# Kernel optimization log

Hardware: AMD Instinct MI355X
Metric: run time of the kernel (lower is better)

The kernel has to match this reference:

```python
import jax, jax.numpy as jnp
import numpy as np
import math

N, E, D, H, EH, DEPTH = 50000, 800000, 128, 128, 16, 3
RATIO = 0.5
BN_SCALE = 1.0 / math.sqrt(1.0 + 1e-5)  # eval-mode BatchNorm1d: running mean 0, var 1
NEG_SLOPE = 0.01  # leaky_relu default


def setup_inputs() -> dict:
    key = jax.random.key(0)
    ks = jax.random.split(key, 16)
    s = lambda k, shape: jax.random.normal(k, shape, dtype=jnp.float32) * 0.05
    return {
        "x": jax.random.normal(ks[0], (N, D), dtype=jnp.float32),
        "edge_index": jax.random.randint(ks[1], (2, E), 0, N, dtype=jnp.int32),
        "edge_attr": jax.random.uniform(ks[2], (E, EH), dtype=jnp.float32),
        "We_w": s(ks[3], (EH, 1)), "We_b": s(ks[4], (1,)),
        "Wdown": s(ks[5], (DEPTH + 1, H, H)), "bdown": s(ks[6], (DEPTH + 1, H)),
        "Wpool": s(ks[7], (DEPTH, H)),
        "Wup": s(ks[8], (DEPTH, H, H)), "bup": s(ks[9], (DEPTH, H)),
        "gnorm": 1.0 + s(ks[10], (DEPTH + 1, H)), "bnorm": s(ks[11], (DEPTH + 1, H)),
        "Wr": s(ks[12], (D, D)), "br": s(ks[13], (D,)),
        "gr": 1.0 + s(ks[14], (D,)), "brn": s(ks[15], (D,)),
    }


def _bn(x, g, b):
    # eval-mode BatchNorm1d with running_mean=0, running_var=1
    return x * (g * BN_SCALE) + b


def _lrelu(x):
    return jnp.where(x > 0, x, NEG_SLOPE * x)


def _gcn(x, src, dst, w, W, b, fill):
    # PyG GCNConv: add self-loops (fill=1.0, improved -> 2.0), symmetric norm
    n = x.shape[0]
    h = x @ W  # [n, H]
    deg = jax.ops.segment_sum(w, dst, num_segments=n) + fill
    dinv = jax.lax.rsqrt(deg)
    coef = dinv[src] * w * dinv[dst]  # [E]
    agg = jax.ops.segment_sum(coef[:, None] * h[src], dst, num_segments=n)
    return agg + (fill / deg)[:, None] * h + b  # self-loop norm = fill/deg


def _topk_pool(x, src, dst, w, p, k):
    # PyG TopKPooling: score = tanh(x.p/||p||), keep top-k, scale kept x by score,
    # filter edges to kept nodes (masked edges kept at fixed length with weight 0)
    n = x.shape[0]
    score = jnp.tanh((x @ p) / jnp.linalg.norm(p))
    vals, perm = jax.lax.top_k(score, k)
    xp = x[perm] * vals[:, None]
    pos = jnp.full((n,), -1, dtype=jnp.int32).at[perm].set(jnp.arange(k, dtype=jnp.int32))
    ns, nd = pos[src], pos[dst]
    valid = (ns >= 0) & (nd >= 0)
    return (xp, jnp.where(valid, ns, 0), jnp.where(valid, nd, 0),
            jnp.where(valid, w, 0.0), perm)


def reference(x, edge_index, edge_attr, We_w, We_b, Wdown, bdown, Wpool, Wup, bup,
              gnorm, bnorm, Wr, br, gr, brn):
    src, dst = edge_index[0], edge_index[1]
    # edge embedding + min/max normalization
    ew = edge_attr @ We_w[:, 0] + We_b[0]  # [E]
    ew = ew - jnp.min(ew)
    ew = ew / (jnp.max(ew) + 1e-7)
    h = _bn(x, gnorm[0], bnorm[0])
    h = _lrelu(_gcn(h, src, dst, ew, Wdown[0], bdown[0], 1.0))
    xs, es, perms = [h], [(src, dst, ew)], []
    for i in range(DEPTH):
        k = int(math.ceil(RATIO * h.shape[0]))
        h, src, dst, ew, perm = _topk_pool(h, src, dst, ew, Wpool[i], k)
        h = _bn(h, gnorm[i + 1], bnorm[i + 1])
        h = _gcn(h, src, dst, ew, Wdown[i + 1], bdown[i + 1], 1.0)
        if i < DEPTH - 1:
            h = _lrelu(h)
            xs.append(h)
            es.append((src, dst, ew))
        perms.append(perm)
    for i in range(DEPTH):
        j = DEPTH - 1 - i
        res = xs[j]
        src, dst, ew = es[j]
        up = jnp.zeros_like(res).at[perms[j]].set(h)  # scatter unpool
        h = _gcn(res + up, src, dst, ew, Wup[i], bup[i], 2.0)  # improved=True -> fill 2
        if i < DEPTH - 1:
            h = _lrelu(h)
    g = jnp.sum(h, axis=0, keepdims=True)  # global_add_pool, single graph
    g = g @ Wr + br
    return _bn(g, gr, brn)
```

## Files before the change

kernel.cpp:

```cpp
#include <hip/hip_runtime.h>
#include <math.h>

#define N0   50000
#define E0   800000
#define HD   128
#define EHD  16
#define KP1  25000
#define KP2  12500
#define KP3  6250
#define BN_SCALE 0.9999950000374997f
#define NEG_SLOPE 0.01f
#define E1C  400000
#define E2C  120000
#define E3C  40000
#define NBE  782
#define CSB  782

#define NBIN   782
#define SBCAP  448
#define OVFCAP 4096

typedef int   vi4 __attribute__((ext_vector_type(4)));
typedef float vf4 __attribute__((ext_vector_type(4)));

__device__ __forceinline__ unsigned fenc(float f) {
    unsigned u = __float_as_uint(f);
    return (u & 0x80000000u) ? ~u : (u | 0x80000000u);
}
__device__ __forceinline__ unsigned packbf2(float a, float b) {
    unsigned ua = __float_as_uint(a);
    unsigned ub = __float_as_uint(b);
    ua = (ua + 0x7FFFu + ((ua >> 16) & 1u)) >> 16;
    ub = (ub + 0x7FFFu + ((ub >> 16) & 1u)) >> 16;
    return ua | (ub << 16);
}
__device__ __forceinline__ void bf8_fma(float* acc, uint4 h, float c) {
    acc[0] += c * __uint_as_float(h.x << 16);
    acc[1] += c * __uint_as_float(h.x & 0xFFFF0000u);
    acc[2] += c * __uint_as_float(h.y << 16);
    acc[3] += c * __uint_as_float(h.y & 0xFFFF0000u);
    acc[4] += c * __uint_as_float(h.z << 16);
    acc[5] += c * __uint_as_float(h.z & 0xFFFF0000u);
    acc[6] += c * __uint_as_float(h.w << 16);
    acc[7] += c * __uint_as_float(h.w & 0xFFFF0000u);
}

__global__ void k_edge_ew(const float* __restrict__ ea, const float* __restrict__ Ww,
                          const float* __restrict__ Wb, float* __restrict__ ew,
                          float2* __restrict__ partials, int E) {
    int e = blockIdx.x * 256 + threadIdx.x;
    float mn = 3.4e38f, mx = -3.4e38f;
    if (e < E) {
        const float4* a4 = (const float4*)(ea + (size_t)e * EHD);
        float s = Wb[0];
        #pragma unroll
        for (int q = 0; q < 4; ++q) {
            float4 a = a4[q];
            s += a.x * Ww[q*4+0] + a.y * Ww[q*4+1] + a.z * Ww[q*4+2] + a.w * Ww[q*4+3];
        }
        ew[e] = s;
        mn = s; mx = s;
    }
    #pragma unroll
    for (int off = 32; off > 0; off >>= 1) {
        mn = fminf(mn, __shfl_xor(mn, off));
        mx = fmaxf(mx, __shfl_xor(mx, off));
    }
    __shared__ float smn[4], smx[4];
    int lane = threadIdx.x & 63, wid = threadIdx.x >> 6;
    if (lane == 0) { smn[wid] = mn; smx[wid] = mx; }
    __syncthreads();
    if (threadIdx.x == 0) {
        float a = fminf(fminf(smn[0], smn[1]), fminf(smn[2], smn[3]));
        float b = fmaxf(fmaxf(smx[0], smx[1]), fmaxf(smx[2], smx[3]));
        partials[blockIdx.x] = make_float2(a, b);
    }
}

__global__ void __launch_bounds__(1024)
k_reduce_mm(const float2* __restrict__ partials, int nb, float* __restrict__ mmv) {
    float mn = 3.4e38f, mx = -3.4e38f;
    for (int i = threadIdx.x; i < nb; i += 1024) {
        float2 t = partials[i];
        mn = fminf(mn, t.x); mx = fmaxf(mx, t.y);
    }
    #pragma unroll
    for (int off = 32; off > 0; off >>= 1) {
        mn = fminf(mn, __shfl_xor(mn, off));
        mx = fmaxf(mx, __shfl_xor(mx, off));
    }
    __shared__ float smn[16], smx[16];
    int lane = threadIdx.x & 63, wid = threadIdx.x >> 6;
    if (lane == 0) { smn[wid] = mn; smx[wid] = mx; }
    __syncthreads();
    if (threadIdx.x == 0) {
        for (int w = 1; w < 16; ++w) { mn = fminf(mn, smn[w]); mx = fmaxf(mx, smx[w]); }
        mmv[0] = mn; mmv[1] = mx;
    }
}

__global__ void __launch_bounds__(256)
k_ew_norm_stage(float* __restrict__ ew, const float* __restrict__ mmv,
                const int* __restrict__ src, const int* __restrict__ dst,
                int* __restrict__ subCnt, uint2* __restrict__ staging,
                int4* __restrict__ ovfList, int* __restrict__ ovfCnt, int E) {
    unsigned xcd;
    asm volatile("s_getreg_b32 %0, hwreg(HW_REG_XCC_ID)" : "=s"(xcd));
    int e = blockIdx.x * 256 + threadIdx.x;
    if (e >= E) return;
    float mn = mmv[0];
    float sc = 1.0f / ((mmv[1] - mn) + 1e-7f);
    float w = (ew[e] - mn) * sc;
    ew[e] = w;
    if (w == 0.0f) return;
    int d = dst[e];
    int s = src[e];
    int sb = (int)xcd * NBIN + (d >> 6);
    int slot = atomicAdd(&subCnt[sb], 1);
    if (slot < SBCAP) {
        staging[(size_t)sb * SBCAP + slot] =
            make_uint2((unsigned)s | ((unsigned)(d & 63) << 16), __float_as_uint(w));
    } else {
        int o = atomicAdd(ovfCnt, 1);
        if (o < OVFCAP) ovfList[o] = make_int4(s, d, __float_as_int(w), 0);
    }
}

__global__ void __launch_bounds__(1024)
k_bin_scan(const int* __restrict__ subCnt, int* __restrict__ binBase,
           int* __restrict__ rowptrEnd) {
    int t = threadIdx.x;
    int v = 0;
    if (t < NBIN) {
        #pragma unroll
        for (int x = 0; x < 8; ++x) v += subCnt[x * NBIN + t];
    }
    int lane = t & 63, wid = t >> 6;
    int xs = v;
    #pragma unroll
    for (int off = 1; off < 64; off <<= 1) {
        int y = __shfl_up(xs, off);
        if (lane >= off) xs += y;
    }
    __shared__ int wsum[16];
    if (lane == 63) wsum[wid] = xs;
    __syncthreads();
    int wb = 0;
    for (int w = 0; w < wid; ++w) wb += wsum[w];
    int excl = wb + xs - v;
    if (t < NBIN) binBase[t] = excl;
    if (t == NBIN - 1) rowptrEnd[0] = excl + v;
}

#define GT_ROWS 64
__global__ void __launch_bounds__(256)
k_gemm128(const float* __restrict__ A, const float* __restrict__ W,
          unsigned* __restrict__ Cb, int n,
          const float* __restrict__ gs, const float* __restrict__ gb,
          const float* __restrict__ up_h, const int* __restrict__ up_pos) {
    __shared__ float As[GT_ROWS][132];
    int tid = threadIdx.x;
    int row0 = blockIdx.x * GT_ROWS;
    int maxr = n - row0;
    {
        #pragma unroll
        for (int it = 0; it < 8; ++it) {
            int idx = it * 256 + tid;
            int r = idx >> 5, q = idx & 31;
            float4 v = make_float4(0.f, 0.f, 0.f, 0.f);
            if (r < maxr) {
                v = ((const float4*)(A + (size_t)(row0 + r) * HD))[q];
                if (up_pos) {
                    int sl = up_pos[row0 + r];
                    if (sl >= 0) {
                        float4 u = ((const float4*)(up_h + (size_t)sl * HD))[q];
                        v.x += u.x; v.y += u.y; v.z += u.z; v.w += u.w;
                    }
                }
                if (gs) {
                    float4 g4 = ((const float4*)gs)[q];
                    float4 b4 = ((const float4*)gb)[q];
                    v.x = v.x * (g4.x * BN_SCALE) + b4.x;
                    v.y = v.y * (g4.y * BN_SCALE) + b4.y;
                    v.z = v.z * (g4.z * BN_SCALE) + b4.z;
                    v.w = v.w * (g4.w * BN_SCALE) + b4.w;
                }
            }
            *(float4*)&As[r][q * 4] = v;
        }
    }
    __syncthreads();
    int cg = tid & 31;
    int rg = tid >> 5;
    float4 acc[8];
    #pragma unroll
    for (int j = 0; j < 8; ++j) acc[j] = make_float4(0.f, 0.f, 0.f, 0.f);
    const float4* W4 = (const float4*)W;
    #pragma unroll 4
    for (int k = 0; k < HD; k += 4) {
        float4 w0 = W4[(k + 0) * 32 + cg];
        float4 w1 = W4[(k + 1) * 32 + cg];
        float4 w2 = W4[(k + 2) * 32 + cg];
        float4 w3 = W4[(k + 3) * 32 + cg];
        #pragma unroll
        for (int jj = 0; jj < 4; ++jj) {
            float4 a = *(const float4*)&As[4 * rg + jj][k];
            acc[jj].x += a.x * w0.x + a.y * w1.x + a.z * w2.x + a.w * w3.x;
            acc[jj].y += a.x * w0.y + a.y * w1.y + a.z * w2.y + a.w * w3.y;
            acc[jj].z += a.x * w0.z + a.y * w1.z + a.z * w2.z + a.w * w3.z;
            acc[jj].w += a.x * w0.w + a.y * w1.w + a.z * w2.w + a.w * w3.w;
        }
        #pragma unroll
        for (int jj = 0; jj < 4; ++jj) {
            float4 a = *(const float4*)&As[32 + 4 * rg + jj][k];
            acc[4 + jj].x += a.x * w0.x + a.y * w1.x + a.z * w2.x + a.w * w3.x;
            acc[4 + jj].y += a.x * w0.y + a.y * w1.y + a.z * w2.y + a.w * w3.y;
            acc[4 + jj].z += a.x * w0.z + a.y * w1.z + a.z * w2.z + a.w * w3.z;
            acc[4 + jj].w += a.x * w0.w + a.y * w1.w + a.z * w2.w + a.w * w3.w;
        }
    }
    #pragma unroll
    for (int jj = 0; jj < 4; ++jj) {
        int r = 4 * rg + jj;
        if (r < maxr) {
            uint2 pk = make_uint2(packbf2(acc[jj].x, acc[jj].y), packbf2(acc[jj].z, acc[jj].w));
            ((uint2*)(Cb + (size_t)(row0 + r) * 64))[cg] = pk;
        }
    }
    #pragma unroll
    for (int jj = 0; jj < 4; ++jj) {
        int r = 32 + 4 * rg + jj;
        if (r < maxr) {
            uint2 pk = make_uint2(packbf2(acc[4+jj].x, acc[4+jj].y), packbf2(acc[4+jj].z, acc[4+jj].w));
            ((uint2*)(Cb + (size_t)(row0 + r) * 64))[cg] = pk;
        }
    }
}

__global__ void k_sum_scan(const int* __restrict__ cnt, int* __restrict__ bsum, int n,
                           int* __restrict__ totalOut, unsigned* __restrict__ dctr) {
    int base = blockIdx.x * 1024;
    int s = 0;
    #pragma unroll
    for (int it = 0; it < 4; ++it) {
        int i = base + it * 256 + threadIdx.x;
        if (i < n) s += cnt[i];
    }
    __shared__ int ws[4];
    __shared__ int lastFlag;
    int lane = threadIdx.x & 63, wid = threadIdx.x >> 6;
    #pragma unroll
    for (int off = 32; off > 0; off >>= 1) s += __shfl_down(s, off);
    if (lane == 0) ws[wid] = s;
    __syncthreads();
    if (threadIdx.x == 0) {
        __hip_atomic_store(&bsum[blockIdx.x], ws[0] + ws[1] + ws[2] + ws[3],
                           __ATOMIC_RELAXED, __HIP_MEMORY_SCOPE_AGENT);
        unsigned prev = __hip_atomic_fetch_add(dctr, 1u, __ATOMIC_ACQ_REL, __HIP_MEMORY_SCOPE_AGENT);
        lastFlag = (prev == gridDim.x - 1);
    }
    __syncthreads();
    if (!lastFlag) return;
    if (threadIdx.x < 64) {
        int nb = gridDim.x;
        int t = threadIdx.x;
        int v = (t < nb) ? __hip_atomic_load(&bsum[t], __ATOMIC_RELAXED, __HIP_MEMORY_SCOPE_AGENT) : 0;
        int x = v;
        #pragma unroll
        for (int off = 1; off < 64; off <<= 1) {
            int y = __shfl_up(x, off);
            if (t >= off) x += y;
        }
        if (t < nb) bsum[t] = x - v;
        if (t == nb - 1) totalOut[0] = x;
    }
    if (threadIdx.x == 0)
        __hip_atomic_store(dctr, 0u, __ATOMIC_RELAXED, __HIP_MEMORY_SCOPE_AGENT);
}

__global__ void k_chunk_scan(const int* __restrict__ cnt, const int* __restrict__ bo,
                             int* __restrict__ rowptr, int* __restrict__ cursor, int n) {
    __shared__ int wsum[4];
    __shared__ int running;
    int base = blockIdx.x * 1024;
    if (threadIdx.x == 0) running = bo[blockIdx.x];
    __syncthreads();
    int lane = threadIdx.x & 63, wid = threadIdx.x >> 6;
    #pragma unroll
    for (int it = 0; it < 4; ++it) {
        int i = base + it * 256 + threadIdx.x;
        int v = (i < n) ? cnt[i] : 0;
        int x = v;
        #pragma unroll
        for (int off = 1; off < 64; off <<= 1) {
            int y = __shfl_up(x, off);
            if (lane >= off) x += y;
        }
        if (lane == 63) wsum[wid] = x;
        __syncthreads();
        int wb = 0;
        for (int w = 0; w < wid; ++w) wb += wsum[w];
        int excl = running + wb + x - v;
        if (i < n) { rowptr[i] = excl; cursor[i] = excl; }
        __syncthreads();
        if (threadIdx.x == 0) running += wsum[0] + wsum[1] + wsum[2] + wsum[3];
        __syncthreads();
    }
}

__global__ void k_csr_fill(const int* __restrict__ src, const int* __restrict__ dst,
                           const float* __restrict__ w, int* __restrict__ cursor,
                           int2* __restrict__ csr,
                           const int* __restrict__ EinPtr, int EinImm) {
    int Ein = EinPtr ? EinPtr[0] : EinImm;
    int e = blockIdx.x * 256 + threadIdx.x;
    if (e >= Ein) return;
    float wv = w[e];
    if (wv == 0.0f) return;
    int slot = atomicAdd(&cursor[dst[e]], 1);
    csr[slot] = make_int2(src[e], __float_as_int(wv));
}

__global__ void __launch_bounds__(256)
k_binB_r(const int* __restrict__ binBase, const int* __restrict__ subCnt,
         const uint2* __restrict__ staging, int2* __restrict__ csr,
         int* __restrict__ cursor, float* __restrict__ sumW,
         int* __restrict__ rowptr, int n) {
    __shared__ int   lhist[64];
    __shared__ int   lcur[64];
    __shared__ float lw[64];
    __shared__ int2  img[2048];
    __shared__ int   segc[8];
    __shared__ int   totalSh;
    int b = blockIdx.x;
    int v0 = b * 64;
    int base = binBase[b];
    if (threadIdx.x < 64) { lhist[threadIdx.x] = 0; lw[threadIdx.x] = 0.f; }
    if (threadIdx.x < 8) segc[threadIdx.x] = min(subCnt[threadIdx.x * NBIN + b], SBCAP);
    __syncthreads();
    #pragma unroll 1
    for (int x = 0; x < 8; ++x) {
        int cnt = segc[x];
        const uint2* st = staging + (size_t)(x * NBIN + b) * SBCAP;
        for (int i = threadIdx.x; i < cnt; i += 256) {
            uint2 en = st[i];
            int dloc = (en.x >> 16) & 63;
            atomicAdd(&lhist[dloc], 1);
            atomicAdd(&lw[dloc], __uint_as_float(en.y));
        }
    }
    __syncthreads();
    if (threadIdx.x < 64) {
        int c = lhist[threadIdx.x];
        int xs = c;
        #pragma unroll
        for (int off = 1; off < 64; off <<= 1) {
            int y = __shfl_up(xs, off);
            if (threadIdx.x >= (unsigned)off) xs += y;
        }
        int excl = xs - c;
        lcur[threadIdx.x] = excl;
        int v = v0 + threadIdx.x;
        if (v < n) { rowptr[v] = base + excl; sumW[v] = lw[threadIdx.x]; }
        if (threadIdx.x == 63) totalSh = xs;
    }
    __syncthreads();
    #pragma unroll 1
    for (int x = 0; x < 8; ++x) {
        int cnt = segc[x];
        const uint2* st = staging + (size_t)(x * NBIN + b) * SBCAP;
        for (int i = threadIdx.x; i < cnt; i += 256) {
            uint2 en = st[i];
            int dloc = (en.x >> 16) & 63;
            int slot = atomicAdd(&lcur[dloc], 1);
            if (slot < 2048) img[slot] = make_int2((int)(en.x & 0xFFFFu), (int)en.y);
        }
    }
    __syncthreads();
    int total = min(totalSh, 2048);
    for (int i = threadIdx.x; i < total; i += 256)
        csr[base + i] = img[i];
    if (threadIdx.x < 64) {
        int v = v0 + threadIdx.x;
        if (v < n) cursor[v] = base + lcur[threadIdx.x];
    }
}

__global__ void k_binOvf(const int4* __restrict__ ovfList, const int* __restrict__ ovfCnt,
                         int* __restrict__ cursor, int2* __restrict__ csr,
                         float* __restrict__ sumW) {
    int cnt = min(ovfCnt[0], OVFCAP);
    for (int i = threadIdx.x; i < cnt; i += 256) {
        int4 e = ovfList[i];
        int slot = atomicAdd(&cursor[e.y], 1);
        csr[slot] = make_int2(e.x, e.z);
        atomicAdd(&sumW[e.y], __int_as_float(e.z));
    }
}

__global__ void k_deg_dinv(const int* __restrict__ rowptr, const int2* __restrict__ csr,
                           float fill, float* __restrict__ deg, float* __restrict__ dinv, int n) {
    int v = blockIdx.x * 256 + threadIdx.x;
    if (v >= n) return;
    float s = fill;
    int rs = rowptr[v], re = rowptr[v + 1];
    for (int j = rs; j < re; ++j) s += __int_as_float(csr[j].y);
    deg[v] = s;
    dinv[v] = rsqrtf(s);
}

__global__ void k_deg_dinv_d(const float* __restrict__ sumW, float fill,
                             float* __restrict__ deg, float* __restrict__ dinv, int n) {
    int v = blockIdx.x * 256 + threadIdx.x;
    if (v >= n) return;
    float s = fill + sumW[v];
    deg[v] = s;
    dinv[v] = rsqrtf(s);
}

__global__ void __launch_bounds__(256)
k_gcn_gather(const int* __restrict__ rowptr, const int2* __restrict__ csr,
             const float* __restrict__ deg, const float* __restrict__ dinv,
             const unsigned* __restrict__ hWb,
             const float* __restrict__ bias,
             float fill, int n, int lrelu, float* __restrict__ out) {
    int v = blockIdx.x * 4 + (threadIdx.x >> 6);
    int lane = threadIdx.x & 63;
    if (v >= n) return;
    int rs = rowptr[v], re = rowptr[v + 1];
    float dv = dinv[v];
    int quarter = lane >> 4;
    int qi = lane & 15;
    float acc[8];
    #pragma unroll
    for (int i = 0; i < 8; ++i) acc[i] = 0.f;
    for (int base = rs; base < re; base += 64) {
        int idx = base + lane;
        int s_r = 0; float c_r = 0.f;
        if (idx < re) {
            int2 ent = csr[idx];
            s_r = ent.x;
            c_r = dinv[s_r] * __int_as_float(ent.y) * dv;
        }
        int cnt = min(64, re - base);
        int groups = cnt >> 2;
        int t = 0;
        for (; t + 1 < groups; t += 2) {
            int j0 = 4 * t + quarter, j1 = j0 + 4;
            int   s0 = __shfl(s_r, j0); float c0 = __shfl(c_r, j0);
            int   s1 = __shfl(s_r, j1); float c1 = __shfl(c_r, j1);
            uint4 h0 = ((const uint4*)(hWb + (size_t)s0 * 64))[qi];
            uint4 h1 = ((const uint4*)(hWb + (size_t)s1 * 64))[qi];
            bf8_fma(acc, h0, c0);
            bf8_fma(acc, h1, c1);
        }
        for (; t < groups; ++t) {
            int j = 4 * t + quarter;
            int s = __shfl(s_r, j); float c = __shfl(c_r, j);
            uint4 h = ((const uint4*)(hWb + (size_t)s * 64))[qi];
            bf8_fma(acc, h, c);
        }
        int rem = cnt & 3;
        if (quarter < rem) {
            int j = groups * 4 + quarter;
            int s = __shfl(s_r, j); float c = __shfl(c_r, j);
            uint4 h = ((const uint4*)(hWb + (size_t)s * 64))[qi];
            bf8_fma(acc, h, c);
        }
    }
    #pragma unroll
    for (int i = 0; i < 8; ++i) {
        acc[i] += __shfl_xor(acc[i], 16);
        acc[i] += __shfl_xor(acc[i], 32);
    }
    if (quarter == 0) {
        uint4 hs = ((const uint4*)(hWb + (size_t)v * 64))[qi];
        float sc = fill / deg[v];
        float hv[8];
        hv[0] = __uint_as_float(hs.x << 16); hv[1] = __uint_as_float(hs.x & 0xFFFF0000u);
        hv[2] = __uint_as_float(hs.y << 16); hv[3] = __uint_as_float(hs.y & 0xFFFF0000u);
        hv[4] = __uint_as_float(hs.z << 16); hv[5] = __uint_as_float(hs.z & 0xFFFF0000u);
        hv[6] = __uint_as_float(hs.w << 16); hv[7] = __uint_as_float(hs.w & 0xFFFF0000u);
        float4 b0 = ((const float4*)bias)[2 * qi];
        float4 b1 = ((const float4*)bias)[2 * qi + 1];
        float o[8];
        o[0] = acc[0] + sc * hv[0] + b0.x;
        o[1] = acc[1] + sc * hv[1] + b0.y;
        o[2] = acc[2] + sc * hv[2] + b0.z;
        o[3] = acc[3] + sc * hv[3] + b0.w;
        o[4] = acc[4] + sc * hv[4] + b1.x;
        o[5] = acc[5] + sc * hv[5] + b1.y;
        o[6] = acc[6] + sc * hv[6] + b1.z;
        o[7] = acc[7] + sc * hv[7] + b1.w;
        if (lrelu) {
            #pragma unroll
            for (int i = 0; i < 8; ++i) o[i] = (o[i] > 0.f) ? o[i] : NEG_SLOPE * o[i];
        }
        float4* orow = (float4*)(out + (size_t)v * HD);
        orow[2 * qi]     = make_float4(o[0], o[1], o[2], o[3]);
        orow[2 * qi + 1] = make_float4(o[4], o[5], o[6], o[7]);
    }
}

__global__ void k_score(const float* __restrict__ x, const float* __restrict__ p,
                        float* __restrict__ score, int n, int* __restrict__ selws) {
    for (int i = blockIdx.x * 256 + threadIdx.x; i < 5120; i += gridDim.x * 256) selws[i] = 0;
    int lane = threadIdx.x & 63;
    float pv0 = p[lane], pv1 = p[lane + 64];
    float ps = pv0 * pv0 + pv1 * pv1;
    #pragma unroll
    for (int off = 32; off > 0; off >>= 1) ps += __shfl_xor(ps, off);
    float rnorm = 1.0f / sqrtf(ps);
    int node = blockIdx.x * 4 + (threadIdx.x >> 6);
    if (node >= n) return;
    const float* row = x + (size_t)node * HD;
    float s = row[lane] * pv0 + row[lane + 64] * pv1;
    #pragma unroll
    for (int off = 32; off > 0; off >>= 1) s += __shfl_xor(s, off);
    if (lane == 0) score[node] = tanhf(s * rnorm);
}

__global__ void __launch_bounds__(256)
k_histpick(const float* __restrict__ score, int n, int pass,
           unsigned* __restrict__ prefix, int* __restrict__ hist,
           int kImm, const int* __restrict__ remIn, int* __restrict__ remOut,
           unsigned* __restrict__ doneCtr) {
    __shared__ int lh[2048];
    int nbins = (pass == 2) ? 1024 : 2048;
    for (int i = threadIdx.x; i < nbins; i += 256) lh[i] = 0;
    __syncthreads();
    unsigned pfx = (pass != 0) ? prefix[0] : 0u;
    int stride = gridDim.x * 256;
    for (int i = blockIdx.x * 256 + threadIdx.x; i < n; i += stride) {
        unsigned u = fenc(score[i]);
        int bin; bool ok;
        if (pass == 0)      { bin = u >> 21;            ok = true; }
        else if (pass == 1) { bin = (u >> 10) & 2047;   ok = ((u >> 21) == (pfx >> 21)); }
        else                { bin = u & 1023;           ok = ((u >> 10) == (pfx >> 10)); }
        if (ok) atomicAdd(&lh[bin], 1);
    }
    __syncthreads();
    for (int i = threadIdx.x; i < nbins; i += 256) {
        int c = lh[i];
        if (c) __hip_atomic_fetch_add(&hist[i], c, __ATOMIC_RELAXED, __HIP_MEMORY_SCOPE_AGENT);
    }
    __syncthreads();
    __shared__ int lastFlag;
    if (threadIdx.x == 0) {
        unsigned prev = __hip_atomic_fetch_add(doneCtr, 1u, __ATOMIC_ACQ_REL, __HIP_MEMORY_SCOPE_AGENT);
        lastFlag = (prev == gridDim.x - 1);
    }
    __syncthreads();
    if (!lastFlag) return;
    __shared__ int wsum[4];
    int k = remIn ? remIn[0] : kImm;
    int t = threadIdx.x;
    int per = nbins >> 8;
    int hi = nbins - t * per, lo = hi - per;
    int s = 0;
    for (int b = lo; b < hi; ++b)
        s += __hip_atomic_load(&hist[b], __ATOMIC_RELAXED, __HIP_MEMORY_SCOPE_AGENT);
    int lane = t & 63, wid = t >> 6;
    int x = s;
    #pragma unroll
    for (int off = 1; off < 64; off <<= 1) {
        int y = __shfl_up(x, off);
        if (lane >= off) x += y;
    }
    if (lane == 63) wsum[wid] = x;
    __syncthreads();
    int wb = 0;
    for (int w = 0; w < wid; ++w) wb += wsum[w];
    int excl = wb + x - s;
    if (k > excl && k <= excl + s) {
        int cum = excl;
        int shift = (pass == 0) ? 21 : (pass == 1) ? 10 : 0;
        for (int b = hi - 1; b >= lo; --b) {
            int h = __hip_atomic_load(&hist[b], __ATOMIC_RELAXED, __HIP_MEMORY_SCOPE_AGENT);
            if (k <= cum + h) {
                unsigned base = (pass == 0) ? 0u : prefix[0];
                prefix[0] = base | ((unsigned)b << shift);
                remOut[0] = k - cum;
                break;
            }
            cum += h;
        }
    }
    __syncthreads();
    if (threadIdx.x == 0)
        __hip_atomic_store(doneCtr, 0u, __ATOMIC_RELAXED, __HIP_MEMORY_SCOPE_AGENT);
}

__global__ void k_cmp_countscan(const float* __restrict__ score, int n,
                                const unsigned* __restrict__ prefix,
                                int* __restrict__ bgt, int* __restrict__ beq,
                                unsigned* __restrict__ dctr) {
    unsigned T = prefix[0];
    int base = blockIdx.x * 1024;
    int gt = 0, eq = 0;
    #pragma unroll
    for (int it = 0; it < 4; ++it) {
        int i = base + it * 256 + threadIdx.x;
        if (i < n) {
            unsigned u = fenc(score[i]);
            gt += (u > T); eq += (u == T);
        }
    }
    __shared__ int sg[4], se[4];
    __shared__ int lastFlag;
    int lane = threadIdx.x & 63, wid = threadIdx.x >> 6;
    #pragma unroll
    for (int off = 32; off > 0; off >>= 1) { gt += __shfl_down(gt, off); eq += __shfl_down(eq, off); }
    if (lane == 0) { sg[wid] = gt; se[wid] = eq; }
    __syncthreads();
    if (threadIdx.x == 0) {
        __hip_atomic_store(&bgt[blockIdx.x], sg[0] + sg[1] + sg[2] + sg[3],
                           __ATOMIC_RELAXED, __HIP_MEMORY_SCOPE_AGENT);
        __hip_atomic_store(&beq[blockIdx.x], se[0] + se[1] + se[2] + se[3],
                           __ATOMIC_RELAXED, __HIP_MEMORY_SCOPE_AGENT);
        unsigned prev = __hip_atomic_fetch_add(dctr, 1u, __ATOMIC_ACQ_REL, __HIP_MEMORY_SCOPE_AGENT);
        lastFlag = (prev == gridDim.x - 1);
    }
    __syncthreads();
    if (!lastFlag) return;
    if (threadIdx.x < 64) {
        int nb = gridDim.x;
        int t = threadIdx.x;
        int va = (t < nb) ? __hip_atomic_load(&bgt[t], __ATOMIC_RELAXED, __HIP_MEMORY_SCOPE_AGENT) : 0;
        int vb = (t < nb) ? __hip_atomic_load(&beq[t], __ATOMIC_RELAXED, __HIP_MEMORY_SCOPE_AGENT) : 0;
        int xa = va, xb = vb;
        #pragma unroll
        for (int off = 1; off < 64; off <<= 1) {
            int ya = __shfl_up(xa, off), yb = __shfl_up(xb, off);
            if (t >= off) { xa += ya; xb += yb; }
        }
        if (t < nb) { bgt[t] = xa - va; beq[t] = xb - vb; }
    }
    if (threadIdx.x == 0)
        __hip_atomic_store(dctr, 0u, __ATOMIC_RELAXED, __HIP_MEMORY_SCOPE_AGENT);
}

__global__ void k_cmp_assign(const float* __restrict__ score, int n, int kcap,
                             const unsigned* __restrict__ prefix,
                             const int* __restrict__ selTies,
                             const int* __restrict__ bgt, const int* __restrict__ beq,
                             int* __restrict__ pos, int* __restrict__ perm,
                             float* __restrict__ vals) {
    unsigned T = prefix[0];
    int tiesNeed = selTies[0];
    __shared__ int wgt[4], weq[4];
    __shared__ int rgt, req;
    int base = blockIdx.x * 1024;
    if (threadIdx.x == 0) { rgt = bgt[blockIdx.x]; req = beq[blockIdx.x]; }
    __syncthreads();
    int lane = threadIdx.x & 63, wid = threadIdx.x >> 6;
    #pragma unroll
    for (int it = 0; it < 4; ++it) {
        int i = base + it * 256 + threadIdx.x;
        bool in = i < n;
        float sc = in ? score[i] : 0.f;
        unsigned u = in ? fenc(sc) : 0u;
        bool g = in && (u > T);
        bool e = in && (u == T);
        unsigned long long mg = __ballot(g), me = __ballot(e);
        int lgt = __popcll(mg & ((1ull << lane) - 1ull));
        int leq = __popcll(me & ((1ull << lane) - 1ull));
        if (lane == 0) { wgt[wid] = __popcll(mg); weq[wid] = __popcll(me); }
        __syncthreads();
        int wbg = 0, wbe = 0;
        for (int w = 0; w < wid; ++w) { wbg += wgt[w]; wbe += weq[w]; }
        int gtRank = rgt + wbg + lgt;
        int tieRank = req + wbe + leq;
        if (in) {
            int slot = -1;
            if (g) slot = gtRank + min(tieRank, tiesNeed);
            else if (e && tieRank < tiesNeed) slot = gtRank + tieRank;
            if (slot >= kcap) slot = -1;
            pos[i] = slot;
            if (slot >= 0) { perm[slot] = i; vals[slot] = sc; }
        }
        __syncthreads();
        if (threadIdx.x == 0) {
            rgt += wgt[0] + wgt[1] + wgt[2] + wgt[3];
            req += weq[0] + weq[1] + weq[2] + weq[3];
        }
        __syncthreads();
    }
}

__global__ void k_pool_bn(const float* __restrict__ x, const int* __restrict__ perm,
                          const float* __restrict__ vals, const float* __restrict__ g,
                          const float* __restrict__ b, float* __restrict__ out, int k) {
    int idx = blockIdx.x * 256 + threadIdx.x;
    if (idx >= k * HD) return;
    int slot = idx >> 7, c = idx & 127;
    int v = perm[slot];
    out[idx] = (x[(size_t)v * HD + c] * vals[slot]) * (g[c] * BN_SCALE) + b[c];
}

__global__ void k_ecompact_countscan(const int* __restrict__ src, const int* __restrict__ dst,
                                     const float* __restrict__ w, const int* __restrict__ pos,
                                     const int* __restrict__ EinPtr, int EinImm, int kNodes,
                                     int* __restrict__ bsumE, int* __restrict__ ecntOut,
                                     int* __restrict__ cnt, unsigned* __restrict__ dctr) {
    int Ein = EinPtr ? EinPtr[0] : EinImm;
    for (int i = blockIdx.x * 256 + threadIdx.x; i < kNodes; i += gridDim.x * 256) cnt[i] = 0;
    int base = blockIdx.x * 1024;
    int c = 0;
    #pragma unroll
    for (int it = 0; it < 4; ++it) {
        int e = base + it * 256 + threadIdx.x;
        if (e < Ein) {
            float wv = w[e];
            if (wv != 0.0f && pos[src[e]] >= 0 && pos[dst[e]] >= 0) ++c;
        }
    }
    __shared__ int ws[4];
    __shared__ int lastFlag;
    int lane = threadIdx.x & 63, wid = threadIdx.x >> 6;
    #pragma unroll
    for (int off = 32; off > 0; off >>= 1) c += __shfl_down(c, off);
    if (lane == 0) ws[wid] = c;
    __syncthreads();
    if (threadIdx.x == 0) {
        __hip_atomic_store(&bsumE[blockIdx.x], ws[0] + ws[1] + ws[2] + ws[3],
                           __ATOMIC_RELAXED, __HIP_MEMORY_SCOPE_AGENT);
        unsigned prev = __hip_atomic_fetch_add(dctr, 1u, __ATOMIC_ACQ_REL, __HIP_MEMORY_SCOPE_AGENT);
        lastFlag = (prev == gridDim.x - 1);
    }
    __syncthreads();
    if (!lastFlag) return;
    {
        __shared__ int wtot[4];
        int nb = gridDim.x;
        int t = threadIdx.x;
        int i0 = t * 4;
        int v0 = (i0 + 0 < nb) ? __hip_atomic_load(&bsumE[i0 + 0], __ATOMIC_RELAXED, __HIP_MEMORY_SCOPE_AGENT) : 0;
        int v1 = (i0 + 1 < nb) ? __hip_atomic_load(&bsumE[i0 + 1], __ATOMIC_RELAXED, __HIP_MEMORY_SCOPE_AGENT) : 0;
        int v2 = (i0 + 2 < nb) ? __hip_atomic_load(&bsumE[i0 + 2], __ATOMIC_RELAXED, __HIP_MEMORY_SCOPE_AGENT) : 0;
        int v3 = (i0 + 3 < nb) ? __hip_atomic_load(&bsumE[i0 + 3], __ATOMIC_RELAXED, __HIP_MEMORY_SCOPE_AGENT) : 0;
        int tot = v0 + v1 + v2 + v3;
        int x2 = tot;
        #pragma unroll
        for (int off = 1; off < 64; off <<= 1) {
            int y = __shfl_up(x2, off);
            if (lane >= off) x2 += y;
        }
        if (lane == 63) wtot[wid] = x2;
        __syncthreads();
        int wb = 0;
        for (int q = 0; q < wid; ++q) wb += wtot[q];
        int excl = wb + x2 - tot;
        if (i0 + 0 < nb) bsumE[i0 + 0] = excl;
        if (i0 + 1 < nb) bsumE[i0 + 1] = excl + v0;
        if (i0 + 2 < nb) bsumE[i0 + 2] = excl + v0 + v1;
        if (i0 + 3 < nb) bsumE[i0 + 3] = excl + v0 + v1 + v2;
        if (t == 255) ecntOut[0] = wtot[0] + wtot[1] + wtot[2] + wtot[3];
    }
    __syncthreads();
    if (threadIdx.x == 0)
        __hip_atomic_store(dctr, 0u, __ATOMIC_RELAXED, __HIP_MEMORY_SCOPE_AGENT);
}

__global__ void k_ecompact_assign(const int* __restrict__ src, const int* __restrict__ dst,
                                  const float* __restrict__ w, const int* __restrict__ pos,
                                  const int* __restrict__ EinPtr, int EinImm,
                                  const int* __restrict__ bsumE,
                                  int* __restrict__ nsrc, int* __restrict__ ndst,
                                  float* __restrict__ nw, int* __restrict__ cnt) {
    int Ein = EinPtr ? EinPtr[0] : EinImm;
    __shared__ int wcnt[4];
    __shared__ int running;
    if (threadIdx.x == 0) running = bsumE[blockIdx.x];
    __syncthreads();
    int base = blockIdx.x * 1024;
    int lane = threadIdx.x & 63, wid = threadIdx.x >> 6;
    #pragma unroll
    for (int it = 0; it < 4; ++it) {
        int e = base + it * 256 + threadIdx.x;
        bool valid = false; int ns = 0, nd = 0; float wv = 0.f;
        if (e < Ein) {
            wv = w[e];
            if (wv != 0.0f) {
                ns = pos[src[e]]; nd = pos[dst[e]];
                valid = (ns >= 0) && (nd >= 0);
            }
        }
        unsigned long long m = __ballot(valid);
        int r = __popcll(m & ((1ull << lane) - 1ull));
        if (lane == 0) wcnt[wid] = __popcll(m);
        __syncthreads();
        int wb = 0;
        for (int w2 = 0; w2 < wid; ++w2) wb += wcnt[w2];
        if (valid) {
            int slot = running + wb + r;
            nsrc[slot] = ns; ndst[slot] = nd; nw[slot] = wv;
            atomicAdd(&cnt[nd], 1);
        }
        __syncthreads();
        if (threadIdx.x == 0) running += wcnt[0] + wcnt[1] + wcnt[2] + wcnt[3];
        __syncthreads();
    }
}

__global__ void __launch_bounds__(256)
k_colsum_part(const float* __restrict__ h, float* __restrict__ cpart, int n) {
    int c = threadIdx.x & 127;
    int rh = threadIdx.x >> 7;
    int r0 = blockIdx.x * 64;
    int r1 = min(n, r0 + 64);
    float local = 0.f;
    for (int r = r0 + rh; r < r1; r += 2) local += h[(size_t)r * HD + c];
    __shared__ float sh[256];
    sh[threadIdx.x] = local;
    __syncthreads();
    if (threadIdx.x < 128) cpart[(size_t)blockIdx.x * HD + c] = sh[c] + sh[c + 128];
}

__global__ void __launch_bounds__(1024)
k_colsum_final(const float* __restrict__ cpart, int nb,
               const float* __restrict__ Wr, const float* __restrict__ br,
               const float* __restrict__ gr, const float* __restrict__ brn,
               float* __restrict__ out) {
    __shared__ float gsh[HD];
    int c = threadIdx.x & 127;
    int seg = threadIdx.x >> 7;
    float local = 0.f;
    for (int b = seg; b < nb; b += 8) local += cpart[(size_t)b * HD + c];
    __shared__ float sh[1024];
    sh[threadIdx.x] = local;
    __syncthreads();
    if (threadIdx.x < 128) {
        float s = 0.f;
        #pragma unroll
        for (int q = 0; q < 8; ++q) s += sh[c + q * 128];
        gsh[c] = s;
    }
    __syncthreads();
    if (threadIdx.x < 128) {
        float s = br[c];
        for (int k = 0; k < HD; ++k) s += gsh[k] * Wr[k * HD + c];
        out[c] = s * (gr[c] * BN_SCALE) + brn[c];
    }
}

extern "C" void kernel_launch(void* const* d_in, const int* in_sizes, int n_in,
                              void* d_out, int out_size, void* d_ws, size_t ws_size,
                              hipStream_t stream) {
    const float* x     = (const float*)d_in[0];
    const int*   ei    = (const int*)d_in[1];
    const float* eattr = (const float*)d_in[2];
    const float* We_w  = (const float*)d_in[3];
    const float* We_b  = (const float*)d_in[4];
    const float* Wdown = (const float*)d_in[5];
    const float* bdown = (const float*)d_in[6];
    const float* Wpool = (const float*)d_in[7];
    const float* Wup   = (const float*)d_in[8];
    const float* bup   = (const float*)d_in[9];
    const float* gnorm = (const float*)d_in[10];
    const float* bnorm = (const float*)d_in[11];
    const float* Wr    = (const float*)d_in[12];
    const float* br    = (const float*)d_in[13];
    const float* gr    = (const float*)d_in[14];
    const float* brn   = (const float*)d_in[15];
    const int* src0 = ei;
    const int* dst0 = ei + E0;
    float* out = (float*)d_out;

    char* p = (char*)d_ws;
    auto alloc = [&](size_t bytes) -> void* {
        void* r = (void*)p;
        p += (bytes + 255) & ~(size_t)255;
        return r;
    };
    float* ew0  = (float*)alloc(E0 * 4);
    int* src1 = (int*)alloc(E1C * 4); int* dst1 = (int*)alloc(E1C * 4); float* ew1 = (float*)alloc(E1C * 4);
    int* src2 = (int*)alloc(E2C * 4); int* dst2 = (int*)alloc(E2C * 4); float* ew2 = (float*)alloc(E2C * 4);
    int* src3 = (int*)alloc(E3C * 4); int* dst3 = (int*)alloc(E3C * 4); float* ew3 = (float*)alloc(E3C * 4);
    float* hbuf = (float*)alloc((size_t)N0 * HD * 4);
    unsigned* hWb = (unsigned*)alloc((size_t)N0 * 64 * 4);
    float* tmp  = (float*)alloc((size_t)N0 * HD * 4);
    float* xs0  = (float*)alloc((size_t)N0 * HD * 4);
    float* xs1  = (float*)alloc((size_t)KP1 * HD * 4);
    float* xs2  = (float*)alloc((size_t)KP2 * HD * 4);
    float* deg   = (float*)alloc(N0 * 4);
    float* dinv  = (float*)alloc(N0 * 4);
    float* sumW0 = (float*)alloc(N0 * 4);
    float* score = (float*)alloc(N0 * 4);
    int*   pos1  = (int*)alloc(N0 * 4);
    int*   pos2  = (int*)alloc(N0 * 4);
    int*   pos3  = (int*)alloc(N0 * 4);
    float* vals  = (float*)alloc(KP1 * 4);
    int* perm1 = (int*)alloc(KP1 * 4);
    int* perm2 = (int*)alloc(KP2 * 4);
    int* perm3 = (int*)alloc(KP3 * 4);
    int* rowptr0 = (int*)alloc((N0 + 1) * 4);
    int* rowptr1 = (int*)alloc((KP1 + 1) * 4);
    int* rowptr2 = (int*)alloc((KP2 + 1) * 4);
    int* rowptr3 = (int*)alloc((KP3 + 1) * 4);
    int2* csrP0 = (int2*)alloc((size_t)E0 * 8);
    int2* csrP1 = (int2*)alloc((size_t)E1C * 8);
    int2* csrP2 = (int2*)alloc((size_t)E2C * 8);
    int2* csrP3 = (int2*)alloc((size_t)E3C * 8);
    int* cnt    = (int*)alloc(N0 * 4);
    int* cursor = (int*)alloc(N0 * 4);
    int* selws  = (int*)alloc(5120 * 4);
    int* hist0 = selws;
    int* hist1 = selws + 2048;
    int* hist2 = selws + 4096;
    int* bgt    = (int*)alloc(64 * 4);
    int* beq    = (int*)alloc(64 * 4);
    int* bsum   = (int*)alloc(64 * 4);
    int* bsumE  = (int*)alloc(1024 * 4);
    float2* partials = (float2*)alloc(((E0 + 255) / 256) * 8);
    float* cpart = (float*)alloc((size_t)CSB * HD * 4);
    float* mmv       = (float*)alloc(64);
    unsigned* ctrws  = (unsigned*)alloc(64 * 4);
    unsigned* dctrS  = ctrws + 0;
    unsigned* dctrH  = ctrws + 8;
    unsigned* dctrC  = ctrws + 16;
    unsigned* dctrE  = ctrws + 24;
    unsigned* prefix = (unsigned*)alloc(64);
    int* rem0        = (int*)alloc(64);
    int* rem1        = (int*)alloc(64);
    int* tiesN       = (int*)alloc(64);
    int* ecnt1       = (int*)alloc(64);
    int* ecnt2       = (int*)alloc(64);
    int* ecnt3       = (int*)alloc(64);
    int* subCnt      = (int*)alloc((8 * NBIN + 64) * 4);
    int* ovfCnt      = subCnt + 8 * NBIN;
    int* binBase     = (int*)alloc((NBIN + 1) * 4);
    int4* ovfList    = (int4*)alloc((size_t)OVFCAP * 16);
    uint2* staging   = (uint2*)tmp;

    const int EB = (E0 + 255) / 256;

    auto build_csr = [&](const int* esrc, const int* edst, const float* eww, int n,
                         int* rowptr, int2* csrP,
                         const int* EinPtr, int EinImm, int gridE) {
        int nb = (n + 1023) / 1024;
        k_sum_scan<<<nb, 256, 0, stream>>>(cnt, bsum, n, rowptr + n, dctrS);
        k_chunk_scan<<<nb, 256, 0, stream>>>(cnt, bsum, rowptr, cursor, n);
        k_csr_fill<<<gridE, 256, 0, stream>>>(esrc, edst, eww, cursor, csrP, EinPtr, EinImm);
    };

    auto run_gcn = [&](const float* hin, const int* rowptr, const int2* csrP,
                       const float* sumW,
                       const float* W, const float* bias, float fill, int n, int lrelu,
                       float* outbuf, const float* bn_g, const float* bn_b,
                       const float* up_h, const int* up_pos) {
        k_gemm128<<<(n + GT_ROWS - 1) / GT_ROWS, 256, 0, stream>>>(hin, W, hWb, n, bn_g, bn_b, up_h, up_pos);
        if (sumW)
            k_deg_dinv_d<<<(n + 255) / 256, 256, 0, stream>>>(sumW, fill, deg, dinv, n);
        else
            k_deg_dinv<<<(n + 255) / 256, 256, 0, stream>>>(rowptr, csrP, fill, deg, dinv, n);
        k_gcn_gather<<<(n + 3) / 4, 256, 0, stream>>>(rowptr, csrP, deg, dinv, hWb,
                                                      bias, fill, n, lrelu, outbuf);
    };

    auto run_pool = [&](const float* xin, int n, int k, const float* pvec,
                        const float* g, const float* b,
                        const int* esrc_in, const int* edst_in, const float* ew_in,
                        const int* EinPtr, int EinImm,
                        int* pos, int* perm,
                        int* esrc_out, int* edst_out, float* ew_out, int* ecntOut) {
        int nb = (n + 1023) / 1024;
        k_score<<<(n + 3) / 4, 256, 0, stream>>>(xin, pvec, score, n, selws);
        k_histpick<<<64, 256, 0, stream>>>(score, n, 0, prefix, hist0, k, (const int*)nullptr, rem0, dctrH);
        k_histpick<<<64, 256, 0, stream>>>(score, n, 1, prefix, hist1, 0, rem0, rem1, dctrH);
        k_histpick<<<64, 256, 0, stream>>>(score, n, 2, prefix, hist2, 0, rem1, tiesN, dctrH);
        k_cmp_countscan<<<nb, 256, 0, stream>>>(score, n, prefix, bgt, beq, dctrC);
        k_cmp_assign<<<nb, 256, 0, stream>>>(score, n, k, prefix, tiesN, bgt, beq, pos, perm, vals);
        k_pool_bn<<<((size_t)k * HD + 255) / 256, 256, 0, stream>>>(xin, perm, vals, g, b, hbuf, k);
        k_ecompact_countscan<<<NBE, 256, 0, stream>>>(esrc_in, edst_in, ew_in, pos, EinPtr, EinImm, k,
                                                      bsumE, ecntOut, cnt, dctrE);
        k_ecompact_assign<<<NBE, 256, 0, stream>>>(esrc_in, edst_in, ew_in, pos, EinPtr, EinImm,
                                                   bsumE, esrc_out, edst_out, ew_out, cnt);
    };

    hipMemsetAsync((void*)ctrws, 0, 64 * 4, stream);
    hipMemsetAsync(subCnt, 0, (size_t)(8 * NBIN + 64) * 4, stream);

    k_edge_ew<<<EB, 256, 0, stream>>>(eattr, We_w, We_b, ew0, partials, E0);
    k_reduce_mm<<<1, 1024, 0, stream>>>(partials, EB, mmv);
    k_ew_norm_stage<<<EB, 256, 0, stream>>>(ew0, mmv, src0, dst0, subCnt, staging,
                                            ovfList, ovfCnt, E0);

    k_bin_scan<<<1, 1024, 0, stream>>>(subCnt, binBase, rowptr0 + N0);
    k_binB_r<<<NBIN, 256, 0, stream>>>(binBase, subCnt, staging, csrP0, cursor, sumW0,
                                       rowptr0, N0);
    k_binOvf<<<1, 256, 0, stream>>>(ovfList, ovfCnt, cursor, csrP0, sumW0);

    run_gcn(x, rowptr0, csrP0, sumW0, Wdown, bdown, 1.0f, N0, 1, xs0, gnorm, bnorm, nullptr, nullptr);

    run_pool(xs0, N0, KP1, Wpool, gnorm + HD, bnorm + HD, src0, dst0, ew0,
             (const int*)nullptr, E0, pos1, perm1, src1, dst1, ew1, ecnt1);
    build_csr(src1, dst1, ew1, KP1, rowptr1, csrP1, ecnt1, 0, (E1C + 255) / 256);
    run_gcn(hbuf, rowptr1, csrP1, nullptr, Wdown + 1 * HD * HD, bdown + 1 * HD, 1.0f, KP1, 1, xs1,
            nullptr, nullptr, nullptr, nullptr);

    run_pool(xs1, KP1, KP2, Wpool + HD, gnorm + 2 * HD, bnorm + 2 * HD, src1, dst1, ew1,
             ecnt1, 0, pos2, perm2, src2, dst2, ew2, ecnt2);
    build_csr(src2, dst2, ew2, KP2, rowptr2, csrP2, ecnt2, 0, (E2C + 255) / 256);
    run_gcn(hbuf, rowptr2, csrP2, nullptr, Wdown + 2 * HD * HD, bdown + 2 * HD, 1.0f, KP2, 1, xs2,
            nullptr, nullptr, nullptr, nullptr);

    run_pool(xs2, KP2, KP3, Wpool + 2 * HD, gnorm + 3 * HD, bnorm + 3 * HD, src2, dst2, ew2,
             ecnt2, 0, pos3, perm3, src3, dst3, ew3, ecnt3);
    build_csr(src3, dst3, ew3, KP3, rowptr3, csrP3, ecnt3, 0, (E3C + 255) / 256);
    run_gcn(hbuf, rowptr3, csrP3, nullptr, Wdown + 3 * HD * HD, bdown + 3 * HD, 1.0f, KP3, 0, tmp,
            nullptr, nullptr, nullptr, nullptr);

    run_gcn(xs2, rowptr2, csrP2, nullptr, Wup, bup, 2.0f, KP2, 1, tmp, nullptr, nullptr, tmp, pos3);

    run_gcn(xs1, rowptr1, csrP1, nullptr, Wup + 1 * HD * HD, bup + 1 * HD, 2.0f, KP1, 1, tmp,
            nullptr, nullptr, tmp, pos2);

    run_gcn(xs0, rowptr0, csrP0, sumW0, Wup + 2 * HD * HD, bup + 2 * HD, 2.0f, N0, 0, tmp,
            nullptr, nullptr, tmp, pos1);

    k_colsum_part<<<CSB, 256, 0, stream>>>(tmp, cpart, N0);
    k_colsum_final<<<1, 1024, 0, stream>>>(cpart, CSB, Wr, br, gr, brn, out);
}
```

Baseline: 841.9 us.

## Replace atomic per-XCD binning with block-local counting sort for level-0 CSR build

Replaces the global-atomic staging of level-0 edges into per-XCD sub-bins (with an overflow list) by a two-pass counting sort. Each of 131 blocks sorts its 6144 edges by destination bin in shared memory and writes per-block counts and offsets. A scan kernel sums the 131 per-block counts for each bin, and each bin block then gathers its segments into LDS and builds the CSR rows. This removes global atomic contention, the memset and the overflow kernel. In exchange, the scan now walks 131 rows per bin, and the gather in k_binB2 is a serial per-thread copy loop. Bins with more than 2048 entries are silently truncated.

```diff
diff --git a/kernel.cpp b/kernel.cpp
--- a/kernel.cpp
+++ b/kernel.cpp
@@ -17,8 +17,9 @@
 #define CSB  782
 
 #define NBIN   782
-#define SBCAP  448
-#define OVFCAP 4096
+#define EPB    6144
+#define NBLK   131
+#define NBINP  784
 
 typedef int   vi4 __attribute__((ext_vector_type(4)));
 typedef float vf4 __attribute__((ext_vector_type(4)));
@@ -99,41 +100,81 @@
     }
 }
 
-__global__ void __launch_bounds__(256)
-k_ew_norm_stage(float* __restrict__ ew, const float* __restrict__ mmv,
-                const int* __restrict__ src, const int* __restrict__ dst,
-                int* __restrict__ subCnt, uint2* __restrict__ staging,
-                int4* __restrict__ ovfList, int* __restrict__ ovfCnt, int E) {
-    unsigned xcd;
-    asm volatile("s_getreg_b32 %0, hwreg(HW_REG_XCC_ID)" : "=s"(xcd));
-    int e = blockIdx.x * 256 + threadIdx.x;
-    if (e >= E) return;
+__global__ void __launch_bounds__(1024)
+k_ew_sortA(float* __restrict__ ew, const float* __restrict__ mmv,
+           const int* __restrict__ src, const int* __restrict__ dst,
+           uint2* __restrict__ staging, int* __restrict__ cntM,
+           int* __restrict__ locOffM, int E) {
+    __shared__ uint2 sEnt[EPB];
+    __shared__ int   lhist[NBINP];
+    __shared__ int   sOff[NBINP];
+    __shared__ int   lcur[NBINP];
+    __shared__ int   wtot[16];
+    int t = threadIdx.x;
+    for (int i = t; i < NBINP; i += 1024) lhist[i] = 0;
+    __syncthreads();
     float mn = mmv[0];
     float sc = 1.0f / ((mmv[1] - mn) + 1e-7f);
-    float w = (ew[e] - mn) * sc;
-    ew[e] = w;
-    if (w == 0.0f) return;
-    int d = dst[e];
-    int s = src[e];
-    int sb = (int)xcd * NBIN + (d >> 6);
-    int slot = atomicAdd(&subCnt[sb], 1);
-    if (slot < SBCAP) {
-        staging[(size_t)sb * SBCAP + slot] =
-            make_uint2((unsigned)s | ((unsigned)(d & 63) << 16), __float_as_uint(w));
-    } else {
-        int o = atomicAdd(ovfCnt, 1);
-        if (o < OVFCAP) ovfList[o] = make_int4(s, d, __float_as_int(w), 0);
-    }
+    int base = blockIdx.x * EPB;
+    unsigned entx[6], enty[6];
+    int bin6[6];
+    #pragma unroll
+    for (int it = 0; it < 6; ++it) {
+        int e = base + it * 1024 + t;
+        bin6[it] = -1;
+        if (e < E) {
+            float w = (ew[e] - mn) * sc;
+            ew[e] = w;
+            if (w != 0.0f) {
+                int d = dst[e];
+                bin6[it] = d >> 6;
+                entx[it] = (unsigned)src[e] | ((unsigned)(d & 63) << 16);
+                enty[it] = __float_as_uint(w);
+                atomicAdd(&lhist[bin6[it]], 1);
+            }
+        }
+    }
+    __syncthreads();
+    {
+        int v = (t < NBINP) ? lhist[t] : 0;
+        int lane = t & 63, wid = t >> 6;
+        int x = v;
+        #pragma unroll
+        for (int off = 1; off < 64; off <<= 1) {
+            int y = __shfl_up(x, off);
+            if (lane >= off) x += y;
+        }
+        if (lane == 63) wtot[wid] = x;
+        __syncthreads();
+        int wb = 0;
+        for (int w = 0; w < wid; ++w) wb += wtot[w];
+        int excl = wb + x - v;
+        if (t < NBINP) { sOff[t] = excl; lcur[t] = excl; }
+    }
+    __syncthreads();
+    #pragma unroll
+    for (int it = 0; it < 6; ++it) {
+        if (bin6[it] >= 0) {
+            int slot = atomicAdd(&lcur[bin6[it]], 1);
+            sEnt[slot] = make_uint2(entx[it], enty[it]);
+        }
+    }
+    __syncthreads();
+    int total = sOff[NBIN];
+    uint2* dstS = staging + (size_t)blockIdx.x * EPB;
+    for (int i = t; i < total; i += 1024) dstS[i] = sEnt[i];
+    int* cRow = cntM + blockIdx.x * NBINP;
+    int* oRow = locOffM + blockIdx.x * NBINP;
+    for (int i = t; i < NBINP; i += 1024) { cRow[i] = lhist[i]; oRow[i] = sOff[i]; }
 }
 
 __global__ void __launch_bounds__(1024)
-k_bin_scan(const int* __restrict__ subCnt, int* __restrict__ binBase,
-           int* __restrict__ rowptrEnd) {
+k_bin_scan2(const int* __restrict__ cntM, int* __restrict__ binBase,
+            int* __restrict__ rowptrEnd) {
     int t = threadIdx.x;
     int v = 0;
     if (t < NBIN) {
-        #pragma unroll
-        for (int x = 0; x < 8; ++x) v += subCnt[x * NBIN + t];
+        for (int blk = 0; blk < NBLK; ++blk) v += cntM[blk * NBINP + t];
     }
     int lane = t & 63, wid = t >> 6;
     int xs = v;
@@ -150,6 +191,79 @@
     int excl = wb + xs - v;
     if (t < NBIN) binBase[t] = excl;
     if (t == NBIN - 1) rowptrEnd[0] = excl + v;
+}
+
+__global__ void __launch_bounds__(256)
+k_binB2(const int* __restrict__ binBase, const int* __restrict__ cntM,
+        const int* __restrict__ locOffM, const uint2* __restrict__ staging,
+        int2* __restrict__ csr, float* __restrict__ sumW,
+        int* __restrict__ rowptr, int n) {
+    __shared__ uint2 raw[2048];
+    __shared__ int   lhist[64];
+    __shared__ int   lcur[64];
+    __shared__ float lw[64];
+    __shared__ int2  img[2048];
+    __shared__ int   wq[4];
+    __shared__ int   totalSh;
+    int b = blockIdx.x;
+    int t = threadIdx.x;
+    int base = binBase[b];
+    int c = 0, lo = 0;
+    if (t < NBLK) { c = cntM[t * NBINP + b]; lo = locOffM[t * NBINP + b]; }
+    int lane = t & 63, wid = t >> 6;
+    int x = c;
+    #pragma unroll
+    for (int off = 1; off < 64; off <<= 1) {
+        int y = __shfl_up(x, off);
+        if (lane >= off) x += y;
+    }
+    if (lane == 63) wq[wid] = x;
+    if (t < 64) { lhist[t] = 0; lw[t] = 0.f; }
+    __syncthreads();
+    int wb = 0;
+    for (int w = 0; w < wid; ++w) wb += wq[w];
+    int pos = wb + x - c;
+    if (t == 255) totalSh = wb + x;
+    __syncthreads();
+    int total = min(totalSh, 2048);
+    if (t < NBLK && c > 0) {
+        const uint2* st = staging + (size_t)t * EPB + lo;
+        for (int j = 0; j < c; ++j) {
+            int p = pos + j;
+            if (p < 2048) raw[p] = st[j];
+        }
+    }
+    __syncthreads();
+    for (int i = t; i < total; i += 256) {
+        uint2 en = raw[i];
+        int dloc = (en.x >> 16) & 63;
+        atomicAdd(&lhist[dloc], 1);
+        atomicAdd(&lw[dloc], __uint_as_float(en.y));
+    }
+    __syncthreads();
+    if (t < 64) {
+        int cc = lhist[t];
+        int xs = cc;
+        #pragma unroll
+        for (int off = 1; off < 64; off <<= 1) {
+            int y = __shfl_up(xs, off);
+            if (t >= off) xs += y;
+        }
+        int excl = xs - cc;
+        lcur[t] = excl;
+        int v = b * 64 + t;
+        if (v < n) { rowptr[v] = base + excl; sumW[v] = lw[t]; }
+    }
+    __syncthreads();
+    for (int i = t; i < total; i += 256) {
+        uint2 en = raw[i];
+        int dloc = (en.x >> 16) & 63;
+        int slot = atomicAdd(&lcur[dloc], 1);
+        if (slot < 2048) img[slot] = make_int2((int)(en.x & 0xFFFFu), (int)en.y);
+    }
+    __syncthreads();
+    for (int i = t; i < total; i += 256)
+        csr[base + i] = img[i];
 }
 
 #define GT_ROWS 64
@@ -319,83 +433,6 @@
     if (wv == 0.0f) return;
     int slot = atomicAdd(&cursor[dst[e]], 1);
     csr[slot] = make_int2(src[e], __float_as_int(wv));
-}
-
-__global__ void __launch_bounds__(256)
-k_binB_r(const int* __restrict__ binBase, const int* __restrict__ subCnt,
-         const uint2* __restrict__ staging, int2* __restrict__ csr,
-         int* __restrict__ cursor, float* __restrict__ sumW,
-         int* __restrict__ rowptr, int n) {
-    __shared__ int   lhist[64];
-    __shared__ int   lcur[64];
-    __shared__ float lw[64];
-    __shared__ int2  img[2048];
-    __shared__ int   segc[8];
-    __shared__ int   totalSh;
-    int b = blockIdx.x;
-    int v0 = b * 64;
-    int base = binBase[b];
-    if (threadIdx.x < 64) { lhist[threadIdx.x] = 0; lw[threadIdx.x] = 0.f; }
-    if (threadIdx.x < 8) segc[threadIdx.x] = min(subCnt[threadIdx.x * NBIN + b], SBCAP);
-    __syncthreads();
-    #pragma unroll 1
-    for (int x = 0; x < 8; ++x) {
-        int cnt = segc[x];
-        const uint2* st = staging + (size_t)(x * NBIN + b) * SBCAP;
-        for (int i = threadIdx.x; i < cnt; i += 256) {
-            uint2 en = st[i];
-            int dloc = (en.x >> 16) & 63;
-            atomicAdd(&lhist[dloc], 1);
-            atomicAdd(&lw[dloc], __uint_as_float(en.y));
-        }
-    }
-    __syncthreads();
-    if (threadIdx.x < 64) {
-        int c = lhist[threadIdx.x];
-        int xs = c;
-        #pragma unroll
-        for (int off = 1; off < 64; off <<= 1) {
-            int y = __shfl_up(xs, off);
-            if (threadIdx.x >= (unsigned)off) xs += y;
-        }
-        int excl = xs - c;
-        lcur[threadIdx.x] = excl;
-        int v = v0 + threadIdx.x;
-        if (v < n) { rowptr[v] = base + excl; sumW[v] = lw[threadIdx.x]; }
-        if (threadIdx.x == 63) totalSh = xs;
-    }
-    __syncthreads();
-    #pragma unroll 1
-    for (int x = 0; x < 8; ++x) {
-        int cnt = segc[x];
-        const uint2* st = staging + (size_t)(x * NBIN + b) * SBCAP;
-        for (int i = threadIdx.x; i < cnt; i += 256) {
-            uint2 en = st[i];
-            int dloc = (en.x >> 16) & 63;
-            int slot = atomicAdd(&lcur[dloc], 1);
-            if (slot < 2048) img[slot] = make_int2((int)(en.x & 0xFFFFu), (int)en.y);
-        }
-    }
-    __syncthreads();
-    int total = min(totalSh, 2048);
-    for (int i = threadIdx.x; i < total; i += 256)
-        csr[base + i] = img[i];
-    if (threadIdx.x < 64) {
-        int v = v0 + threadIdx.x;
-        if (v < n) cursor[v] = base + lcur[threadIdx.x];
-    }
-}
-
-__global__ void k_binOvf(const int4* __restrict__ ovfList, const int* __restrict__ ovfCnt,
-                         int* __restrict__ cursor, int2* __restrict__ csr,
-                         float* __restrict__ sumW) {
-    int cnt = min(ovfCnt[0], OVFCAP);
-    for (int i = threadIdx.x; i < cnt; i += 256) {
-        int4 e = ovfList[i];
-        int slot = atomicAdd(&cursor[e.y], 1);
-        csr[slot] = make_int2(e.x, e.z);
-        atomicAdd(&sumW[e.y], __int_as_float(e.z));
-    }
 }
 
 __global__ void k_deg_dinv(const int* __restrict__ rowptr, const int2* __restrict__ csr,
@@ -927,10 +964,9 @@
     int* ecnt1       = (int*)alloc(64);
     int* ecnt2       = (int*)alloc(64);
     int* ecnt3       = (int*)alloc(64);
-    int* subCnt      = (int*)alloc((8 * NBIN + 64) * 4);
-    int* ovfCnt      = subCnt + 8 * NBIN;
+    int* cntM        = (int*)alloc((size_t)NBLK * NBINP * 4);
+    int* locOffM     = (int*)alloc((size_t)NBLK * NBINP * 4);
     int* binBase     = (int*)alloc((NBIN + 1) * 4);
-    int4* ovfList    = (int4*)alloc((size_t)OVFCAP * 16);
     uint2* staging   = (uint2*)tmp;
 
     const int EB = (E0 + 255) / 256;
@@ -979,17 +1015,14 @@
     };
 
     hipMemsetAsync((void*)ctrws, 0, 64 * 4, stream);
-    hipMemsetAsync(subCnt, 0, (size_t)(8 * NBIN + 64) * 4, stream);
 
     k_edge_ew<<<EB, 256, 0, stream>>>(eattr, We_w, We_b, ew0, partials, E0);
     k_reduce_mm<<<1, 1024, 0, stream>>>(partials, EB, mmv);
-    k_ew_norm_stage<<<EB, 256, 0, stream>>>(ew0, mmv, src0, dst0, subCnt, staging,
-                                            ovfList, ovfCnt, E0);
-
-    k_bin_scan<<<1, 1024, 0, stream>>>(subCnt, binBase, rowptr0 + N0);
-    k_binB_r<<<NBIN, 256, 0, stream>>>(binBase, subCnt, staging, csrP0, cursor, sumW0,
-                                       rowptr0, N0);
-    k_binOvf<<<1, 256, 0, stream>>>(ovfList, ovfCnt, cursor, csrP0, sumW0);
+    k_ew_sortA<<<NBLK, 1024, 0, stream>>>(ew0, mmv, src0, dst0, staging, cntM, locOffM, E0);
+
+    k_bin_scan2<<<1, 1024, 0, stream>>>(cntM, binBase, rowptr0 + N0);
+    k_binB2<<<NBIN, 256, 0, stream>>>(binBase, cntM, locOffM, staging, csrP0, sumW0,
+                                      rowptr0, N0);
 
     run_gcn(x, rowptr0, csrP0, sumW0, Wdown, bdown, 1.0f, N0, 1, xs0, gnorm, bnorm, nullptr, nullptr);
 
```

Result: no change. 836.4 us (-0.7%).
